# Kernel tuning notes

Hardware: AMD Instinct MI355X
Metric: run time of the kernel (lower is better)

The kernel has to match this reference:

```python
import math
import jax, jax.numpy as jnp
import numpy as np

SR = 22050
FRAME_SIZE = 1025  # n_fft=2048 -> 1025 bins
MAX_FILTER_SIZE = 20
B, T = 32, 2000


def _to_mel(freq):
    return 2595.0 * np.log10(1.0 + freq / 700.0)


def build_transform_matrix(frame_size=FRAME_SIZE, sr=SR, max_filter_size=MAX_FILTER_SIZE):
    # Banded Gaussian smoothing matrix; filter width grows in mel scale (<= max_filter_size).
    freq = np.linspace(0.0, sr / 2.0, num=frame_size, endpoint=True)
    mel = _to_mel(freq)
    raw = (mel - mel[0]) / (mel[-1] - mel[0]) * (max_filter_size - 1) + 1
    mtx = np.zeros((frame_size, frame_size), dtype=np.float64)
    for i in range(frame_size):
        fs = int(math.floor(raw[i])) // 2 * 2 + 1  # odd filter size
        if fs == 1:
            mtx[i, i] = 1.0
            continue
        sigma = (fs - 1) / 6.0
        # replicate scipy.ndimage.gaussian_filter1d (order=0, mode='reflect', truncate=4)
        radius = int(4.0 * sigma + 0.5)
        x = np.arange(-radius, radius + 1)
        k = np.exp(-0.5 * (x / sigma) ** 2)
        k /= k.sum()
        imp = np.zeros(fs)
        imp[fs // 2] = 1.0
        # scipy 'reflect' == numpy 'symmetric'; symmetric kernel so convolve == correlate
        f = np.convolve(np.pad(imp, radius, mode='symmetric'), k, mode='valid')
        start, end = max(0, i - fs // 2), min(i + fs // 2 + 1, frame_size)
        f_start = start - i + fs // 2
        f_end = end - i + fs // 2
        f = f[f_start:f_end]
        mtx[i, start:end] = f / f.sum()
    return mtx.astype(np.float32)


def setup_inputs() -> dict:
    key = jax.random.key(0)
    k1, k2 = jax.random.split(key)
    model_output = jax.random.normal(k1, (B, FRAME_SIZE, T), dtype=jnp.float32)
    target = jax.random.normal(k2, (B, FRAME_SIZE, T), dtype=jnp.float32)
    transform_matrix = jnp.asarray(build_transform_matrix())
    return {"model_output": model_output, "target": target,
            "transform_matrix": transform_matrix}


def reference(model_output, target, transform_matrix):
    # db_to_amp(x) = 10**(x/20); (db_to_amp(x))**2 = 10**(x/10)
    mo = jnp.power(jnp.float32(10.0), model_output / jnp.float32(10.0))
    tg = jnp.power(jnp.float32(10.0), target / jnp.float32(10.0))
    diff = mo - tg  # [B, F, T]
    transformed = jnp.einsum('fk,bkt->bft', transform_matrix, diff)
    return jnp.mean(transformed ** 2)
```

## Files before the change

### kernel.cpp

```cpp
#include <hip/hip_runtime.h>
#include <math.h>


#define B_N 32
#define F_N 1025
#define T_N 2000

#define NOUT   106
#define NCHUNK 10
#define NT     256
#define CT     512
#define CST    24

#define LOG2_10_DIV10 0.33219280948873623f

__global__ __launch_bounds__(NT, 4)
void mel_mse_stream(const float* __restrict__ mo_g, const float* __restrict__ tg_g,
                    const float* __restrict__ M, float* __restrict__ partials) {
    __shared__ float sm[NOUT * CST];
    __shared__ float red[NT];

    const int tid = threadIdx.x;
    const int t0  = blockIdx.x * CT;
    const int f0  = blockIdx.y * NOUT;
    const int b   = blockIdx.z;
    const int t   = t0 + tid * 2;
    const bool active = (t + 1 < T_N);

    for (int i = tid; i < NOUT * 21; i += NT) {
        const int row = i / 21;
        const int j   = i - row * 21;
        const int f   = f0 + row;
        const int k   = f - 10 + j;
        float v = 0.f;
        if (f < F_N && k >= 0 && k < F_N) v = M[(size_t)f * F_N + k];
        sm[row * CST + j] = v;
    }
    __syncthreads();

    const int    tc      = active ? t : 0;
    const size_t colbase = ((size_t)b * F_N) * (size_t)T_N + tc;
    const int    base    = f0 - 10;

    float2 w[21];
    float  acc = 0.f;

    auto LOAD = [&](int r) -> float2 {
        int g = base + r;
        const float mask = (active && g >= 0 && g < F_N) ? 1.f : 0.f;
        g = g < 0 ? 0 : (g >= F_N ? F_N - 1 : g);
        const size_t off = colbase + (size_t)g * T_N;
        const float2 a = *reinterpret_cast<const float2*>(mo_g + off);
        const float2 c = *reinterpret_cast<const float2*>(tg_g + off);
        float2 d;
        d.x = (exp2f(a.x * LOG2_10_DIV10) - exp2f(c.x * LOG2_10_DIV10)) * mask;
        d.y = (exp2f(a.y * LOG2_10_DIV10) - exp2f(c.y * LOG2_10_DIV10)) * mask;
        return d;
    };
    auto OUT = [&](int r_out, int s0) {
        if (f0 + r_out < F_N) {
            const float* c = &sm[r_out * CST];
            float2 o = make_float2(0.f, 0.f);
#pragma unroll
            for (int j = 0; j < 21; ++j) {
                const float  m  = c[j];
                const float2 wv = w[(s0 + j) % 21];
                o.x = fmaf(m, wv.x, o.x);
                o.y = fmaf(m, wv.y, o.y);
            }
            acc = fmaf(o.x, o.x, fmaf(o.y, o.y, acc));
        }
    };

#pragma unroll
    for (int i = 0; i < 21; ++i) w[i] = LOAD(i);
    OUT(0, 0);

    for (int m = 1; m < 6; ++m) {
        const int rb = m * 21;
#pragma unroll
        for (int i = 0; i < 21; ++i) {
            w[i] = LOAD(rb + i);
            OUT(rb + i - 20, (i + 1) % 21);
        }
    }

    red[tid] = acc;
    __syncthreads();
    for (int s = NT / 2; s > 0; s >>= 1) {
        if (tid < s) red[tid] += red[tid + s];
        __syncthreads();
    }
    if (tid == 0) {
        const int bid = blockIdx.x + gridDim.x * (blockIdx.y + gridDim.y * blockIdx.z);
        partials[bid] = red[0];
    }
}

__global__ void mel_mse_reduce(const float* __restrict__ partials, int n,
                               float* __restrict__ out) {
    __shared__ double red[256];
    double s = 0.0;
    for (int i = threadIdx.x; i < n; i += 256) s += (double)partials[i];
    red[threadIdx.x] = s;
    __syncthreads();
    for (int st = 128; st > 0; st >>= 1) {
        if (threadIdx.x < st) red[threadIdx.x] += red[threadIdx.x + st];
        __syncthreads();
    }
    if (threadIdx.x == 0)
        out[0] = (float)(red[0] / (double)((long long)B_N * F_N * T_N));
}

extern "C" void kernel_launch(void* const* d_in, const int* in_sizes, int n_in,
                              void* d_out, int out_size, void* d_ws, size_t ws_size,
                              hipStream_t stream) {
    const float* mo = (const float*)d_in[0];
    const float* tg = (const float*)d_in[1];
    const float* M  = (const float*)d_in[2];
    float* out      = (float*)d_out;
    float* partials = (float*)d_ws;

    dim3 grid((T_N + CT - 1) / CT,
              NCHUNK,
              B_N);
    const int nparts = grid.x * grid.y * grid.z;

    mel_mse_stream<<<grid, NT, 0, stream>>>(mo, tg, M, partials);
    mel_mse_reduce<<<1, 256, 0, stream>>>(partials, nparts, out);
}
```

Before: 131.0 us.

## Shrink row chunks, add unmasked fast path, vectorize filter coefficient loads

Reduces output rows per block from 106 to 64 (17 chunks) and raises the occupancy hint to 5 blocks per CU. Adds a fast path for interior chunks that walks pointers without clamping or masking, and reads shared-memory filter coefficients as float4. The inactive-thread mask moves to a single zeroing at the end. Smaller chunks re-read a larger fraction of halo rows (84 loaded per 64 outputs versus 126 per 106), adding extra global traffic and exp work in exchange for more parallelism and cheaper inner loops.

```diff
diff --git a/kernel.cpp b/kernel.cpp
--- a/kernel.cpp
+++ b/kernel.cpp
@@ -6,15 +6,16 @@
 #define F_N 1025
 #define T_N 2000
 
-#define NOUT   106
-#define NCHUNK 10
+#define NOUT   64
+#define ROWS   84
+#define NCHUNK 17
 #define NT     256
 #define CT     512
 #define CST    24
 
 #define LOG2_10_DIV10 0.33219280948873623f
 
-__global__ __launch_bounds__(NT, 4)
+__global__ __launch_bounds__(NT, 5)
 void mel_mse_stream(const float* __restrict__ mo_g, const float* __restrict__ tg_g,
                     const float* __restrict__ M, float* __restrict__ partials) {
     __shared__ float sm[NOUT * CST];
@@ -26,66 +27,99 @@
     const int b   = blockIdx.z;
     const int t   = t0 + tid * 2;
     const bool active = (t + 1 < T_N);
+    const int base = f0 - 10;
 
-    for (int i = tid; i < NOUT * 21; i += NT) {
-        const int row = i / 21;
-        const int j   = i - row * 21;
+    for (int i = tid; i < NOUT * CST; i += NT) {
+        const int row = i / CST;
+        const int j   = i - row * CST;
         const int f   = f0 + row;
         const int k   = f - 10 + j;
         float v = 0.f;
-        if (f < F_N && k >= 0 && k < F_N) v = M[(size_t)f * F_N + k];
-        sm[row * CST + j] = v;
+        if (j < 21 && f < F_N && k >= 0 && k < F_N) v = M[(size_t)f * F_N + k];
+        sm[i] = v;
     }
     __syncthreads();
 
-    const int    tc      = active ? t : 0;
-    const size_t colbase = ((size_t)b * F_N) * (size_t)T_N + tc;
-    const int    base    = f0 - 10;
+    const int tc = active ? t : 0;
 
     float2 w[21];
-    float  acc = 0.f;
+    float2 acc = make_float2(0.f, 0.f);
 
-    auto LOAD = [&](int r) -> float2 {
-        int g = base + r;
-        const float mask = (active && g >= 0 && g < F_N) ? 1.f : 0.f;
-        g = g < 0 ? 0 : (g >= F_N ? F_N - 1 : g);
-        const size_t off = colbase + (size_t)g * T_N;
-        const float2 a = *reinterpret_cast<const float2*>(mo_g + off);
-        const float2 c = *reinterpret_cast<const float2*>(tg_g + off);
-        float2 d;
-        d.x = (exp2f(a.x * LOG2_10_DIV10) - exp2f(c.x * LOG2_10_DIV10)) * mask;
-        d.y = (exp2f(a.y * LOG2_10_DIV10) - exp2f(c.y * LOG2_10_DIV10)) * mask;
-        return d;
-    };
-    auto OUT = [&](int r_out, int s0) {
-        if (f0 + r_out < F_N) {
-            const float* c = &sm[r_out * CST];
-            float2 o = make_float2(0.f, 0.f);
+    auto OUTF = [&](int r_out, const int s0) {
+        float cf[24];
+        const float4* c4 = reinterpret_cast<const float4*>(&sm[r_out * CST]);
 #pragma unroll
-            for (int j = 0; j < 21; ++j) {
-                const float  m  = c[j];
-                const float2 wv = w[(s0 + j) % 21];
-                o.x = fmaf(m, wv.x, o.x);
-                o.y = fmaf(m, wv.y, o.y);
-            }
-            acc = fmaf(o.x, o.x, fmaf(o.y, o.y, acc));
+        for (int q = 0; q < 6; ++q)
+            *reinterpret_cast<float4*>(&cf[q * 4]) = c4[q];
+        float2 o = make_float2(0.f, 0.f);
+#pragma unroll
+        for (int j = 0; j < 21; ++j) {
+            const float2 wv = w[(s0 + j) % 21];
+            o.x = fmaf(cf[j], wv.x, o.x);
+            o.y = fmaf(cf[j], wv.y, o.y);
         }
+        acc.x = fmaf(o.x, o.x, acc.x);
+        acc.y = fmaf(o.y, o.y, acc.y);
     };
 
+    const bool fast = (base >= 0) && (base + ROWS <= F_N);
+
+    if (fast) {
+        const float* pm = mo_g + ((size_t)b * F_N + base) * (size_t)T_N + tc;
+        const float* pt = tg_g + ((size_t)b * F_N + base) * (size_t)T_N + tc;
+        auto LOADF = [&]() -> float2 {
+            const float2 a = *reinterpret_cast<const float2*>(pm);
+            const float2 c = *reinterpret_cast<const float2*>(pt);
+            pm += T_N; pt += T_N;
+            float2 d;
+            d.x = exp2f(a.x * LOG2_10_DIV10) - exp2f(c.x * LOG2_10_DIV10);
+            d.y = exp2f(a.y * LOG2_10_DIV10) - exp2f(c.y * LOG2_10_DIV10);
+            return d;
+        };
 #pragma unroll
-    for (int i = 0; i < 21; ++i) w[i] = LOAD(i);
-    OUT(0, 0);
-
-    for (int m = 1; m < 6; ++m) {
-        const int rb = m * 21;
+        for (int i = 0; i < 21; ++i) w[i] = LOADF();
+        OUTF(0, 0);
+        for (int m = 1; m < 4; ++m) {
+            const int rb = m * 21;
 #pragma unroll
-        for (int i = 0; i < 21; ++i) {
-            w[i] = LOAD(rb + i);
-            OUT(rb + i - 20, (i + 1) % 21);
+            for (int i = 0; i < 21; ++i) {
+                w[i] = LOADF();
+                OUTF(rb + i - 20, (i + 1) % 21);
+            }
+        }
+    } else {
+        const size_t colbase = ((size_t)b * F_N) * (size_t)T_N + tc;
+        auto LOADS = [&](int r) -> float2 {
+            int g = base + r;
+            const float mask = (g >= 0 && g < F_N) ? 1.f : 0.f;
+            g = g < 0 ? 0 : (g >= F_N ? F_N - 1 : g);
+            const size_t off = colbase + (size_t)g * T_N;
+            const float2 a = *reinterpret_cast<const float2*>(mo_g + off);
+            const float2 c = *reinterpret_cast<const float2*>(tg_g + off);
+            float2 d;
+            d.x = (exp2f(a.x * LOG2_10_DIV10) - exp2f(c.x * LOG2_10_DIV10)) * mask;
+            d.y = (exp2f(a.y * LOG2_10_DIV10) - exp2f(c.y * LOG2_10_DIV10)) * mask;
+            return d;
+        };
+        auto OUTS = [&](int r_out, const int s0) {
+            if (f0 + r_out < F_N) OUTF(r_out, s0);
+        };
+#pragma unroll
+        for (int i = 0; i < 21; ++i) w[i] = LOADS(i);
+        OUTS(0, 0);
+        for (int m = 1; m < 4; ++m) {
+            const int rb = m * 21;
+#pragma unroll
+            for (int i = 0; i < 21; ++i) {
+                w[i] = LOADS(rb + i);
+                OUTS(rb + i - 20, (i + 1) % 21);
+            }
         }
     }
 
-    red[tid] = acc;
+    if (!active) acc = make_float2(0.f, 0.f);
+
+    red[tid] = acc.x + acc.y;
     __syncthreads();
     for (int s = NT / 2; s > 0; s >>= 1) {
         if (tid < s) red[tid] += red[tid + s];
```

After: 297.3 us. 2.27x slower.

## Prefetch rows in a register ring and read band coefficients from a prebuilt global buffer

Applied to the files above, without the earlier changes.

A separate kernel now packs the banded transform matrix into a compact global buffer, so each streaming block no longer fills shared memory and waits on a barrier. The stream kernel processes one column per thread instead of two, doubling the grid, raising the occupancy hint to 8, and software-prefetching the next 7 rows of inputs into registers before consuming them. Coefficients are read with float4 global loads served from cache rather than from shared memory. This adds an extra kernel launch and more global coefficient traffic, and loses the float2 vector loads.

```diff
diff --git a/kernel.cpp b/kernel.cpp
--- a/kernel.cpp
+++ b/kernel.cpp
@@ -7,83 +7,99 @@
 #define T_N 2000
 
 #define NOUT   106
+#define ROWS   126
 #define NCHUNK 10
 #define NT     256
-#define CT     512
-#define CST    24
+#define PF     7
+#define CBS    24
+#define BANDROWS (NCHUNK * NOUT)
 
 #define LOG2_10_DIV10 0.33219280948873623f
 
-__global__ __launch_bounds__(NT, 4)
+__global__ void build_band(const float* __restrict__ M, float* __restrict__ band) {
+    const int idx = blockIdx.x * 256 + threadIdx.x;
+    if (idx >= BANDROWS * CBS) return;
+    const int f = idx / CBS;
+    const int j = idx - f * CBS;
+    const int k = f - 10 + j;
+    float v = 0.f;
+    if (j < 21 && f < F_N && k >= 0 && k < F_N) v = M[(size_t)f * F_N + k];
+    band[idx] = v;
+}
+
+__global__ __launch_bounds__(NT, 8)
 void mel_mse_stream(const float* __restrict__ mo_g, const float* __restrict__ tg_g,
-                    const float* __restrict__ M, float* __restrict__ partials) {
-    __shared__ float sm[NOUT * CST];
+                    const float* __restrict__ band, float* __restrict__ partials) {
     __shared__ float red[NT];
 
-    const int tid = threadIdx.x;
-    const int t0  = blockIdx.x * CT;
-    const int f0  = blockIdx.y * NOUT;
-    const int b   = blockIdx.z;
-    const int t   = t0 + tid * 2;
-    const bool active = (t + 1 < T_N);
+    const int tid  = threadIdx.x;
+    const int t    = blockIdx.x * NT + tid;
+    const int f0   = blockIdx.y * NOUT;
+    const int b    = blockIdx.z;
+    const int base = f0 - 10;
 
-    for (int i = tid; i < NOUT * 21; i += NT) {
-        const int row = i / 21;
-        const int j   = i - row * 21;
-        const int f   = f0 + row;
-        const int k   = f - 10 + j;
-        float v = 0.f;
-        if (f < F_N && k >= 0 && k < F_N) v = M[(size_t)f * F_N + k];
-        sm[row * CST + j] = v;
-    }
-    __syncthreads();
+    const bool colv  = (t < T_N);
+    const int  tc    = colv ? t : 0;
+    const float cmask = colv ? 1.f : 0.f;
 
-    const int    tc      = active ? t : 0;
-    const size_t colbase = ((size_t)b * F_N) * (size_t)T_N + tc;
-    const int    base    = f0 - 10;
+    float w[21];
+    float ra[PF], rc[PF];
+    float rm[PF];
+    float acc = 0.f;
 
-    float2 w[21];
-    float  acc = 0.f;
-
-    auto LOAD = [&](int r) -> float2 {
-        int g = base + r;
-        const float mask = (active && g >= 0 && g < F_N) ? 1.f : 0.f;
-        g = g < 0 ? 0 : (g >= F_N ? F_N - 1 : g);
-        const size_t off = colbase + (size_t)g * T_N;
-        const float2 a = *reinterpret_cast<const float2*>(mo_g + off);
-        const float2 c = *reinterpret_cast<const float2*>(tg_g + off);
-        float2 d;
-        d.x = (exp2f(a.x * LOG2_10_DIV10) - exp2f(c.x * LOG2_10_DIV10)) * mask;
-        d.y = (exp2f(a.y * LOG2_10_DIV10) - exp2f(c.y * LOG2_10_DIV10)) * mask;
-        return d;
+    auto ISSUE = [&](int n, int s) {
+        const int g  = base + n;
+        rm[s] = (g >= 0 && g < F_N) ? 1.f : 0.f;
+        const int gc = g < 0 ? 0 : (g > F_N - 1 ? F_N - 1 : g);
+        const size_t off = ((size_t)b * F_N + gc) * (size_t)T_N + tc;
+        ra[s] = mo_g[off];
+        rc[s] = tg_g[off];
     };
-    auto OUT = [&](int r_out, int s0) {
-        if (f0 + r_out < F_N) {
-            const float* c = &sm[r_out * CST];
-            float2 o = make_float2(0.f, 0.f);
+    auto CONSUME = [&](int s, int ws) {
+        const float d = (exp2f(ra[s] * LOG2_10_DIV10) -
+                         exp2f(rc[s] * LOG2_10_DIV10)) * rm[s];
+        w[ws] = d;
+    };
+    auto OUT = [&](int frow, int s0) {
+        float cf[24];
+        const float4* c4 = reinterpret_cast<const float4*>(band + (size_t)frow * CBS);
 #pragma unroll
-            for (int j = 0; j < 21; ++j) {
-                const float  m  = c[j];
-                const float2 wv = w[(s0 + j) % 21];
-                o.x = fmaf(m, wv.x, o.x);
-                o.y = fmaf(m, wv.y, o.y);
-            }
-            acc = fmaf(o.x, o.x, fmaf(o.y, o.y, acc));
-        }
+        for (int q = 0; q < 6; ++q)
+            *reinterpret_cast<float4*>(&cf[q * 4]) = c4[q];
+        float o = 0.f;
+#pragma unroll
+        for (int j = 0; j < 21; ++j)
+            o = fmaf(cf[j], w[(s0 + j) % 21], o);
+        acc = fmaf(o, o, acc);
     };
 
 #pragma unroll
-    for (int i = 0; i < 21; ++i) w[i] = LOAD(i);
-    OUT(0, 0);
+    for (int i = 0; i < PF; ++i) ISSUE(i, i);
 
-    for (int m = 1; m < 6; ++m) {
-        const int rb = m * 21;
+#pragma unroll
+    for (int i = 0; i < 21; ++i) {
+        CONSUME(i % PF, i);
+        ISSUE(i + PF, i % PF);
+        if (i == 20) OUT(f0, 0);
+    }
+    for (int m = 1; m < 5; ++m) {
+        const int nb = m * 21;
 #pragma unroll
         for (int i = 0; i < 21; ++i) {
-            w[i] = LOAD(rb + i);
-            OUT(rb + i - 20, (i + 1) % 21);
+            CONSUME(i % PF, i);
+            ISSUE(nb + i + PF, i % PF);
+            OUT(f0 + nb + i - 20, (i + 1) % 21);
         }
     }
+#pragma unroll
+    for (int i = 0; i < 21; ++i) {
+        CONSUME(i % PF, i);
+        if (i < ROWS - 105 - PF)
+            ISSUE(105 + i + PF, i % PF);
+        OUT(f0 + 105 + i - 20, (i + 1) % 21);
+    }
+
+    acc *= cmask;
 
     red[tid] = acc;
     __syncthreads();
@@ -118,14 +134,18 @@
     const float* mo = (const float*)d_in[0];
     const float* tg = (const float*)d_in[1];
     const float* M  = (const float*)d_in[2];
-    float* out      = (float*)d_out;
-    float* partials = (float*)d_ws;
 
-    dim3 grid((T_N + CT - 1) / CT,
+    float* out  = (float*)d_out;
+    float* band = (float*)d_ws;
+    float* partials = (float*)((char*)d_ws + 102400);
+
+    build_band<<<(BANDROWS * CBS + 255) / 256, 256, 0, stream>>>(M, band);
+
+    dim3 grid((T_N + NT - 1) / NT,
               NCHUNK,
               B_N);
     const int nparts = grid.x * grid.y * grid.z;
 
-    mel_mse_stream<<<grid, NT, 0, stream>>>(mo, tg, M, partials);
+    mel_mse_stream<<<grid, NT, 0, stream>>>(mo, tg, band, partials);
     mel_mse_reduce<<<1, 256, 0, stream>>>(partials, nparts, out);
 }
```

Measured after the change: 195.1 us. 48.9% more time.
